# Optimization experiments

Hardware: AMD Instinct MI355X
Metric: run time of the kernel (lower is better)

The kernel has to match this reference:

```python
import jax, jax.numpy as jnp
import numpy as np

NSIDE = 64
NPIX = 12 * NSIDE * NSIDE  # hp.nside2npix(64) = 49152
B, C, N = 8, 16, 524288    # C = in_features - 2


def setup_inputs() -> dict:
    key = jax.random.key(0)
    k1, k2 = jax.random.split(key)
    vals = jax.random.normal(k1, (B, C, N), dtype=jnp.float32)
    pix = jax.random.randint(k2, (B, N), 0, NPIX, dtype=jnp.int32)
    return {"vals": vals, "pix": pix}


def reference(vals, pix):
    # Faithful to the torch loop: pooled[b, p, :] += vals[b, 0, i] (scalar from
    # channel 0 broadcast over all C output channels), counts[b, p] += 1,
    # counts clamped to >= 1, then mean.
    b_off = NPIX * jnp.arange(B, dtype=pix.dtype)[:, None]          # [B,1]
    flat_idx = (pix + b_off).reshape(-1)                            # [B*N]
    v0 = vals[:, 0, :].reshape(-1)                                  # [B*N]
    seg = jax.ops.segment_sum(v0, flat_idx, num_segments=B * NPIX)
    cnt = jax.ops.segment_sum(jnp.ones_like(v0), flat_idx, num_segments=B * NPIX)
    seg = seg.reshape(B, NPIX)
    cnt = jnp.maximum(cnt.reshape(B, NPIX), 1.0)
    pooled = jnp.broadcast_to((seg / cnt)[:, :, None], (B, NPIX, C))
    return pooled
```

## Files before the change

### kernel.cpp

```cpp
#include <hip/hip_runtime.h>

#define NSIDE 64
#define NPIX  (12 * NSIDE * NSIDE)
#define BATCH 8
#define CH    16
#define NPTS  524288

#define BIN_SHIFT 7
#define BPB   128
#define BINS  (NPIX / BPB)
#define NBINS (BATCH * BINS)
#define WGS_PER_BATCH 64
#define NWG   (BATCH * WGS_PER_BATCH)
#define SLICE (NPTS / WGS_PER_BATCH)
#define QSCALE 262144.0f
#define QMAX   ((1 << 24) - 1)

#define TBL_STRIDE 512
#define REC_OFFSET (1u << 20)

__global__ __launch_bounds__(256) void hpx_partition(const float* __restrict__ vals,
                                                     const int* __restrict__ pix,
                                                     unsigned int* __restrict__ table,
                                                     unsigned int* __restrict__ rec) {
    __shared__ unsigned int hist[BINS];
    __shared__ unsigned int start[BINS];
    __shared__ unsigned int gsum[24];
    __shared__ unsigned int srec[SLICE];

    const int wg  = blockIdx.x;
    const int b   = wg >> 6;
    const int s   = wg & (WGS_PER_BATCH - 1);
    const int tid = threadIdx.x;

    for (int i = tid; i < BINS; i += 256) hist[i] = 0u;
    __syncthreads();

    const int*   pixb = pix  + (size_t)b * NPTS + (size_t)s * SLICE;
    const float* valb = vals + (size_t)b * (CH * (size_t)NPTS) + (size_t)s * SLICE;

    int4 pr[8];
    unsigned short rank[32];
    #pragma unroll
    for (int it = 0; it < 8; ++it) {
        pr[it] = *(const int4*)(pixb + it * 1024 + tid * 4);
        rank[it * 4 + 0] = (unsigned short)atomicAdd(&hist[pr[it].x >> BIN_SHIFT], 1u);
        rank[it * 4 + 1] = (unsigned short)atomicAdd(&hist[pr[it].y >> BIN_SHIFT], 1u);
        rank[it * 4 + 2] = (unsigned short)atomicAdd(&hist[pr[it].z >> BIN_SHIFT], 1u);
        rank[it * 4 + 3] = (unsigned short)atomicAdd(&hist[pr[it].w >> BIN_SHIFT], 1u);
    }
    __syncthreads();

    if (tid < 24) {
        unsigned int acc = 0;
        #pragma unroll
        for (int k = 0; k < 16; ++k) {
            unsigned int h = hist[tid * 16 + k];
            start[tid * 16 + k] = acc;
            acc += h;
        }
        gsum[tid] = acc;
    }
    __syncthreads();
    if (tid == 0) {
        unsigned int a = 0;
        #pragma unroll
        for (int k = 0; k < 24; ++k) { unsigned int t = gsum[k]; gsum[k] = a; a += t; }
    }
    __syncthreads();
    for (int i = tid; i < BINS; i += 256) start[i] += gsum[i >> 4];
    __syncthreads();

    #pragma unroll
    for (int it = 0; it < 8; ++it) {
        float4 v4 = *(const float4*)(valb + it * 1024 + tid * 4);
        int   p[4] = {pr[it].x, pr[it].y, pr[it].z, pr[it].w};
        float v[4] = {v4.x, v4.y, v4.z, v4.w};
        #pragma unroll
        for (int k = 0; k < 4; ++k) {
            int bin = p[k] >> BIN_SHIFT;
            unsigned int pos = start[bin] + (unsigned int)rank[it * 4 + k];
            int q = (int)lrintf(v[k] * QSCALE);
            q = q > QMAX ? QMAX : (q < -QMAX ? -QMAX : q);
            srec[pos] = ((unsigned int)(p[k] & (BPB - 1)) << 25) | ((unsigned int)q & 0x1FFFFFFu);
        }
    }
    __syncthreads();

    {
        const uint4* s4 = (const uint4*)srec;
        uint4* r4 = (uint4*)(rec + (size_t)wg * SLICE);
        #pragma unroll
        for (int it = 0; it < (SLICE / 4) / 256; ++it)
            r4[it * 256 + tid] = s4[it * 256 + tid];
        for (int i = tid; i < BINS + 1; i += 256)
            table[(size_t)wg * TBL_STRIDE + i] = (i < BINS) ? start[i] : (unsigned int)SLICE;
    }
}

__global__ __launch_bounds__(256) void hpx_reduce(const unsigned int* __restrict__ rec,
                                                  const unsigned int* __restrict__ table,
                                                  float4* __restrict__ out) {
    __shared__ unsigned long long acc[BPB];
    __shared__ float mean[BPB];

    const int wg  = blockIdx.x;
    const int b   = wg / BINS;
    const int bin = wg % BINS;
    const int tid = threadIdx.x;

    if (tid < BPB) acc[tid] = 0ULL;
    __syncthreads();

    const int wave = tid >> 6, lane = tid & 63;
    for (int s = wave; s < WGS_PER_BATCH; s += 4) {
        int srcwg = b * WGS_PER_BATCH + s;
        unsigned int off = table[(size_t)srcwg * TBL_STRIDE + bin];
        unsigned int end = table[(size_t)srcwg * TBL_STRIDE + bin + 1];
        const unsigned int* r = rec + (size_t)srcwg * SLICE;
        for (unsigned int j = off + lane; j < end; j += 64) {
            unsigned int u = r[j];
            unsigned int bkt = u >> 25;
            long long sv = ((int)(u << 7)) >> 7;
            atomicAdd(&acc[bkt], (1ULL << 44) + (unsigned long long)sv);
        }
    }
    __syncthreads();

    if (tid < BPB) {
        unsigned long long a = acc[tid];
        long long sv = ((long long)(a << 20)) >> 20;
        unsigned int c = (unsigned int)((a - (unsigned long long)sv) >> 44);
        mean[tid] = (float)sv * (1.0f / QSCALE) / (float)(c ? c : 1u);
    }
    __syncthreads();

    size_t obase = ((size_t)b * NPIX + (size_t)bin * BPB) * 4;
    #pragma unroll
    for (int q = 0; q < 2; ++q) {
        int idx = q * 256 + tid;
        float m = mean[idx >> 2];
        out[obase + idx] = make_float4(m, m, m, m);
    }
}

#define SUM_SCALE 16777216.0f
#define CNT_SHIFT 44

__global__ void hpx_zero_ws(unsigned long long* __restrict__ accg, int n) {
    int i = blockIdx.x * blockDim.x + threadIdx.x;
    if (i < n) accg[i] = 0ULL;
}

__global__ void hpx_scatter(const float* __restrict__ vals,
                            const int* __restrict__ pix,
                            unsigned long long* __restrict__ accg) {
    int t = blockIdx.x * blockDim.x + threadIdx.x;
    int e0 = t * 4;
    if (e0 >= BATCH * NPTS) return;
    int b = e0 >> 19;
    int j = e0 & (NPTS - 1);
    int4   p4 = *(const int4*)(pix + e0);
    float4 v4 = *(const float4*)(vals + (size_t)b * (CH * (size_t)NPTS) + j);
    const unsigned long long one = 1ULL << CNT_SHIFT;
    int base = b * NPIX;
    long long s0 = (long long)llrintf(v4.x * SUM_SCALE);
    long long s1 = (long long)llrintf(v4.y * SUM_SCALE);
    long long s2 = (long long)llrintf(v4.z * SUM_SCALE);
    long long s3 = (long long)llrintf(v4.w * SUM_SCALE);
    atomicAdd(&accg[base + p4.x], one + (unsigned long long)s0);
    atomicAdd(&accg[base + p4.y], one + (unsigned long long)s1);
    atomicAdd(&accg[base + p4.z], one + (unsigned long long)s2);
    atomicAdd(&accg[base + p4.w], one + (unsigned long long)s3);
}

__global__ void hpx_finalize(const unsigned long long* __restrict__ accg,
                             float4* __restrict__ out) {
    int t = blockIdx.x * blockDim.x + threadIdx.x;
    if (t >= BATCH * NPIX * 4) return;
    int bp = t >> 2;
    unsigned long long a = accg[bp];
    long long s = ((long long)(a << (64 - CNT_SHIFT))) >> (64 - CNT_SHIFT);
    unsigned int c = (unsigned int)((a - (unsigned long long)s) >> CNT_SHIFT);
    float denom = (float)(c > 0u ? c : 1u);
    float m = (float)((double)s * (1.0 / (double)SUM_SCALE)) / denom;
    out[t] = make_float4(m, m, m, m);
}

extern "C" void kernel_launch(void* const* d_in, const int* in_sizes, int n_in,
                              void* d_out, int out_size, void* d_ws, size_t ws_size,
                              hipStream_t stream) {
    const float* vals = (const float*)d_in[0];
    const int*   pix  = (const int*)d_in[1];
    float*       out  = (float*)d_out;

    const size_t need = (size_t)REC_OFFSET + (size_t)NWG * SLICE * sizeof(unsigned int);

    if (ws_size >= need) {
        unsigned int* table = (unsigned int*)d_ws;
        unsigned int* rec   = (unsigned int*)((char*)d_ws + REC_OFFSET);

        hpx_partition<<<NWG, 256, 0, stream>>>(vals, pix, table, rec);
        hpx_reduce<<<NBINS, 256, 0, stream>>>(rec, table, (float4*)out);
    } else {
        const int nbuckets = BATCH * NPIX;
        unsigned long long* accg = (unsigned long long*)d_ws;
        hpx_zero_ws<<<(nbuckets + 255) / 256, 256, 0, stream>>>(accg, nbuckets);
        int total_threads = (BATCH * NPTS) / 4;
        hpx_scatter<<<total_threads / 256, 256, 0, stream>>>(vals, pix, accg);
        int total = BATCH * NPIX * 4;
        hpx_finalize<<<(total + 255) / 256, 256, 0, stream>>>(accg, (float4*)out);
    }
}
```

Measured before the change: 339.8 us.

## Double partition workgroups, prefetch values early, and use 16-lane groups in reduce

The partition stage now splits each batch across 128 workgroups with half-size slices, which raises parallelism and cuts per-block LDS use. Pixel and value loads are issued together up front so they overlap with the histogram atomics. The reduce stage first caches the per-source offset and end values in shared memory, then gives each source slice a 16-lane group instead of a full 64-lane wave. Short per-bin runs should therefore waste fewer lanes, at the cost of twice as many table entries to read per bin.

```diff
diff --git a/kernel.cpp b/kernel.cpp
--- a/kernel.cpp
+++ b/kernel.cpp
@@ -10,14 +10,14 @@
 #define BPB   128
 #define BINS  (NPIX / BPB)
 #define NBINS (BATCH * BINS)
-#define WGS_PER_BATCH 64
+#define WGS_PER_BATCH 128
 #define NWG   (BATCH * WGS_PER_BATCH)
 #define SLICE (NPTS / WGS_PER_BATCH)
 #define QSCALE 262144.0f
 #define QMAX   ((1 << 24) - 1)
 
 #define TBL_STRIDE 512
-#define REC_OFFSET (1u << 20)
+#define REC_OFFSET (1u << 21)
 
 __global__ __launch_bounds__(256) void hpx_partition(const float* __restrict__ vals,
                                                      const int* __restrict__ pix,
@@ -29,7 +29,7 @@
     __shared__ unsigned int srec[SLICE];
 
     const int wg  = blockIdx.x;
-    const int b   = wg >> 6;
+    const int b   = wg >> 7;
     const int s   = wg & (WGS_PER_BATCH - 1);
     const int tid = threadIdx.x;
 
@@ -39,11 +39,17 @@
     const int*   pixb = pix  + (size_t)b * NPTS + (size_t)s * SLICE;
     const float* valb = vals + (size_t)b * (CH * (size_t)NPTS) + (size_t)s * SLICE;
 
-    int4 pr[8];
-    unsigned short rank[32];
-    #pragma unroll
-    for (int it = 0; it < 8; ++it) {
+    int4   pr[4];
+    float4 vr[4];
+    #pragma unroll
+    for (int it = 0; it < 4; ++it) {
         pr[it] = *(const int4*)(pixb + it * 1024 + tid * 4);
+        vr[it] = *(const float4*)(valb + it * 1024 + tid * 4);
+    }
+
+    unsigned short rank[16];
+    #pragma unroll
+    for (int it = 0; it < 4; ++it) {
         rank[it * 4 + 0] = (unsigned short)atomicAdd(&hist[pr[it].x >> BIN_SHIFT], 1u);
         rank[it * 4 + 1] = (unsigned short)atomicAdd(&hist[pr[it].y >> BIN_SHIFT], 1u);
         rank[it * 4 + 2] = (unsigned short)atomicAdd(&hist[pr[it].z >> BIN_SHIFT], 1u);
@@ -72,10 +78,9 @@
     __syncthreads();
 
     #pragma unroll
-    for (int it = 0; it < 8; ++it) {
-        float4 v4 = *(const float4*)(valb + it * 1024 + tid * 4);
+    for (int it = 0; it < 4; ++it) {
         int   p[4] = {pr[it].x, pr[it].y, pr[it].z, pr[it].w};
-        float v[4] = {v4.x, v4.y, v4.z, v4.w};
+        float v[4] = {vr[it].x, vr[it].y, vr[it].z, vr[it].w};
         #pragma unroll
         for (int k = 0; k < 4; ++k) {
             int bin = p[k] >> BIN_SHIFT;
@@ -103,22 +108,31 @@
                                                   float4* __restrict__ out) {
     __shared__ unsigned long long acc[BPB];
     __shared__ float mean[BPB];
+    __shared__ unsigned int roff[WGS_PER_BATCH];
+    __shared__ unsigned int rend[WGS_PER_BATCH];
 
     const int wg  = blockIdx.x;
     const int b   = wg / BINS;
     const int bin = wg % BINS;
     const int tid = threadIdx.x;
+    const int base_srcwg = b * WGS_PER_BATCH;
 
     if (tid < BPB) acc[tid] = 0ULL;
-    __syncthreads();
-
-    const int wave = tid >> 6, lane = tid & 63;
-    for (int s = wave; s < WGS_PER_BATCH; s += 4) {
-        int srcwg = b * WGS_PER_BATCH + s;
-        unsigned int off = table[(size_t)srcwg * TBL_STRIDE + bin];
-        unsigned int end = table[(size_t)srcwg * TBL_STRIDE + bin + 1];
-        const unsigned int* r = rec + (size_t)srcwg * SLICE;
-        for (unsigned int j = off + lane; j < end; j += 64) {
+    if (tid < WGS_PER_BATCH) {
+        roff[tid] = table[(size_t)(base_srcwg + tid) * TBL_STRIDE + bin];
+    } else {
+        rend[tid - WGS_PER_BATCH] =
+            table[(size_t)(base_srcwg + (tid - WGS_PER_BATCH)) * TBL_STRIDE + bin + 1];
+    }
+    __syncthreads();
+
+    const int g = tid >> 4;
+    const int l = tid & 15;
+    for (int s = g; s < WGS_PER_BATCH; s += 16) {
+        unsigned int off = roff[s];
+        unsigned int end = rend[s];
+        const unsigned int* r = rec + (size_t)(base_srcwg + s) * SLICE;
+        for (unsigned int j = off + l; j < end; j += 16) {
             unsigned int u = r[j];
             unsigned int bkt = u >> 25;
             long long sv = ((int)(u << 7)) >> 7;
```

After: 329.0 us. 3.2% less time.
